# Kernel tuning notes

Hardware: AMD Instinct MI355X
Metric: run time of the kernel (lower is better)

The kernel has to match this reference:

```python
import jax, jax.numpy as jnp
import numpy as np

B, T, D, H, P, A = 128, 512, 512, 512, 512, 32  # envs, steps, feat, lstm hidden, latent, actions


def setup_inputs() -> dict:
    key = jax.random.key(0)
    ks = jax.random.split(key, 30)
    N = B * T
    lin = lambda k, o, i: 0.02 * jax.random.normal(k, (o, i), jnp.float32)
    vec = lambda k, o: 0.02 * jax.random.normal(k, (o,), jnp.float32)
    inp = {
        'features': jax.random.normal(ks[0], (N, D), jnp.float32),
        'episode_starts': (jax.random.uniform(ks[1], (N,)) < 0.02).astype(jnp.float32),
        'h0_pi': jax.random.normal(ks[2], (1, B, H), jnp.float32),
        'c0_pi': jax.random.normal(ks[3], (1, B, H), jnp.float32),
        'h0_vf': jax.random.normal(ks[4], (1, B, H), jnp.float32),
        'c0_vf': jax.random.normal(ks[5], (1, B, H), jnp.float32),
        'Wih_pi': lin(ks[6], 4 * H, D), 'Whh_pi': lin(ks[7], 4 * H, H),
        'bih_pi': vec(ks[8], 4 * H), 'bhh_pi': vec(ks[9], 4 * H),
        'Wih_vf': lin(ks[10], 4 * H, D), 'Whh_vf': lin(ks[11], 4 * H, H),
        'bih_vf': vec(ks[12], 4 * H), 'bhh_vf': vec(ks[13], 4 * H),
        'pol_w1': lin(ks[14], P, H), 'pol_b1': vec(ks[15], P),
        'pol_w2': lin(ks[16], P, P), 'pol_b2': vec(ks[17], P),
        'val_w1': lin(ks[18], P, H), 'val_b1': vec(ks[19], P),
        'val_w2': lin(ks[20], P, P), 'val_b2': vec(ks[21], P),
        'actor_w': lin(ks[22], A, P), 'actor_b': vec(ks[23], A),
        'critic_w': lin(ks[24], 1, P), 'critic_b': vec(ks[25], 1),
        'deterministic': 1,
    }
    return inp


def masked_lstm(xs, starts, h0, c0, Wih, Whh, bih, bhh):
    # xs: [T,B,D], starts: [T,B]; PyTorch gate order i,f,g,o; reset h,c where episode starts.
    def step(carry, inp):
        h, c = carry
        x, s = inp
        m = (1.0 - s)[:, None]
        h, c = h * m, c * m
        g = x @ Wih.T + bih + h @ Whh.T + bhh
        i, f, gg, o = jnp.split(g, 4, axis=-1)
        c = jax.nn.sigmoid(f) * c + jax.nn.sigmoid(i) * jnp.tanh(gg)
        h = jax.nn.sigmoid(o) * jnp.tanh(c)
        return (h, c), h
    (hT, cT), ys = jax.lax.scan(step, (h0[0], c0[0]), (xs, starts))
    return ys, hT[None], cT[None]


def mlp(x, w1, b1, w2, b2):
    return jax.nn.relu(x @ w1.T + b1) @ w2.T + b2


def reference(features, episode_starts, h0_pi, c0_pi, h0_vf, c0_vf,
              Wih_pi, Whh_pi, bih_pi, bhh_pi, Wih_vf, Whh_vf, bih_vf, bhh_vf,
              pol_w1, pol_b1, pol_w2, pol_b2, val_w1, val_b1, val_w2, val_b2,
              actor_w, actor_b, critic_w, critic_b, deterministic):
    n_seq = h0_pi.shape[1]
    d = features.shape[-1]
    xs = features.reshape(n_seq, -1, d).swapaxes(0, 1)        # [T,B,D]
    st = episode_starts.reshape(n_seq, -1).swapaxes(0, 1)     # [T,B]
    ys_pi, h_pi, c_pi = masked_lstm(xs, st, h0_pi, c0_pi, Wih_pi, Whh_pi, bih_pi, bhh_pi)
    ys_vf, h_vf, c_vf = masked_lstm(xs, st, h0_vf, c0_vf, Wih_vf, Whh_vf, bih_vf, bhh_vf)
    hsz = ys_pi.shape[-1]
    lat_pi = ys_pi.swapaxes(0, 1).reshape(-1, hsz)            # [B*T,H]
    lat_vf = ys_vf.swapaxes(0, 1).reshape(-1, hsz)
    lat_pi = mlp(lat_pi, pol_w1, pol_b1, pol_w2, pol_b2)
    lat_vf = mlp(lat_vf, val_w1, val_b1, val_w2, val_b2)
    values = lat_vf @ critic_w.T + critic_b                    # [B*T,1]
    logits = lat_pi @ actor_w.T + actor_b                      # [B*T,A]
    actions = jnp.argmax(logits, axis=-1)                      # deterministic mode
    logp = jax.nn.log_softmax(logits, axis=-1)
    log_prob = jnp.take_along_axis(logp, actions[:, None], axis=1)[:, 0]
    return actions, values, log_prob, h_pi, c_pi, h_vf, c_vf
```

## Files before the change

### kernel.cpp

```cpp
#include <hip/hip_runtime.h>
#include <math.h>

#define BB 128
#define TT 512
#define DD 512
#define HH 512
#define NN (BB*TT)
#define PP 512
#define AA 32
#define CH 64
#define CR (BB*CH)

typedef unsigned short u16;
typedef unsigned int   u32;
typedef __attribute__((ext_vector_type(8))) short short8;
typedef __attribute__((ext_vector_type(4))) float f32x4;

__device__ __forceinline__ u16 f2bf(float f){
    u32 x = __float_as_uint(f);
    u32 r = (x + 0x7fffu + ((x >> 16) & 1u)) >> 16;
    return (u16)r;
}
__device__ __forceinline__ float bf2f(u16 u){
    return __uint_as_float(((u32)u) << 16);
}
__device__ __forceinline__ f32x4 mfma16(short8 a, short8 b, f32x4 c){
    return __builtin_amdgcn_mfma_f32_16x16x32_bf16(a, b, c, 0, 0, 0);
}
__device__ __forceinline__ float sigm(float x){
    return 1.f/(1.f + __expf(-x));
}
__device__ __forceinline__ float tanh_f(float x){
    return 1.f - 2.f/(1.f + __expf(2.f*x));
}

__device__ __forceinline__ short8 ld_mall(const u16* p){
    short8 r;
    asm volatile("global_load_dwordx4 %0, %1, off sc0 sc1"
                 : "=&v"(r) : "v"(p) : "memory");
    return r;
}
__device__ __forceinline__ void st_mall(u16* p, short8 v){
    asm volatile("global_store_dwordx4 %0, %1, off sc0 sc1"
                 :: "v"(p), "v"(v) : "memory");
}

__device__ __forceinline__ unsigned a_add(unsigned* p){
    return __hip_atomic_fetch_add(p, 1u, __ATOMIC_RELAXED, __HIP_MEMORY_SCOPE_AGENT);
}
__device__ __forceinline__ unsigned a_ld(unsigned* p){
    return __hip_atomic_load(p, __ATOMIC_RELAXED, __HIP_MEMORY_SCOPE_AGENT);
}

#define BARZ_N 75264

__global__ __launch_bounds__(256) void prep_lstm_w(
    const float* __restrict__ Wih_pi, const float* __restrict__ Whh_pi,
    const float* __restrict__ bih_pi, const float* __restrict__ bhh_pi,
    const float* __restrict__ Wih_vf, const float* __restrict__ Whh_vf,
    const float* __restrict__ bih_vf, const float* __restrict__ bhh_vf,
    u16* __restrict__ wihHi, u16* __restrict__ wihLo,
    u16* __restrict__ whhHi, u16* __restrict__ whhLo,
    float* __restrict__ biasP)
{
    long i = (long)blockIdx.x*256 + threadIdx.x;
    if (i >= 2L*2048*512) return;
    int L = (int)(i >> 20);
    int rem = (int)(i & 1048575);
    int c = rem >> 9, k = rem & 511;
    int u = c >> 2, g = c & 3;
    long src = (long)(g*512 + u)*512 + k;
    float wih = (L ? Wih_vf : Wih_pi)[src];
    float whh = (L ? Whh_vf : Whh_pi)[src];
    u16 h1 = f2bf(wih); wihHi[i] = h1; wihLo[i] = f2bf(wih - bf2f(h1));
    u16 h2 = f2bf(whh); whhHi[i] = h2; whhLo[i] = f2bf(whh - bf2f(h2));
    if (k == 0) {
        float b = (L ? bih_vf : bih_pi)[g*512+u] + (L ? bhh_vf : bhh_pi)[g*512+u];
        biasP[L*2048 + c] = b;
    }
}

__global__ __launch_bounds__(256) void prep_mlp_w(
    const float* __restrict__ w1pi, const float* __restrict__ w1vf,
    const float* __restrict__ w2pi, const float* __restrict__ w2vf,
    const float* __restrict__ b1pi, const float* __restrict__ b1vf,
    const float* __restrict__ b2pi, const float* __restrict__ b2vf,
    u16* __restrict__ mHi, u16* __restrict__ mLo, float* __restrict__ biasM)
{
    long i = (long)blockIdx.x*256 + threadIdx.x;
    if (i >= 4L*262144) return;
    int mat = (int)(i >> 18);
    int rem = (int)(i & 262143);
    const float* src = mat==0 ? w1pi : mat==1 ? w1vf : mat==2 ? w2pi : w2vf;
    float v = src[rem];
    u16 h = f2bf(v); mHi[i] = h; mLo[i] = f2bf(v - bf2f(h));
    if (rem < 512) {
        const float* bs = mat==0 ? b1pi : mat==1 ? b1vf : mat==2 ? b2pi : b2vf;
        biasM[mat*512 + rem] = bs[rem];
    }
}

__global__ __launch_bounds__(256) void init_state_k(
    const float* __restrict__ h0_pi, const float* __restrict__ c0_pi,
    const float* __restrict__ h0_vf, const float* __restrict__ c0_vf,
    const float* __restrict__ starts,
    u16* __restrict__ hHi, u16* __restrict__ hLo, float* __restrict__ cT,
    float* __restrict__ startsT, unsigned* __restrict__ barZ)
{
    int i = blockIdx.x*256 + threadIdx.x;
    if (i < BARZ_N) barZ[i] = 0u;
    if (i < NN) {
        int e = i >> 9, t = i & 511;
        startsT[t*128 + e] = starts[i];
    }
    if (i >= 2*BB*HH) return;
    int L = i >> 16; int r = i & 65535;
    int e = r >> 9, u = r & 511;
    float m = 1.0f - starts[(long)e*TT];
    float h = (L ? h0_vf : h0_pi)[r] * m;
    float c = (L ? c0_vf : c0_pi)[r] * m;
    long hidx = (long)(L*2)*65536 + r;
    u16 hh = f2bf(h);
    hHi[hidx] = hh; hLo[hidx] = f2bf(h - bf2f(hh));
    cT[(long)L*65536 + (long)u*128 + e] = c;
}

template<int AM, int EM>
__global__ __launch_bounds__(256) void gemm_k512(
    const float* __restrict__ Afp,
    const u16* __restrict__ aHi, const u16* __restrict__ aLo, long aZ,
    int rowSh, int rowOuterHi, int rowOuterLo, int rowBase,
    const u16* __restrict__ bHi, const u16* __restrict__ bLo, long bZ,
    const float* __restrict__ bias, long biasZ,
    float* __restrict__ outF, long outFZ, int outLd,
    u16* __restrict__ oHi, u16* __restrict__ oLo, long oZ)
{
    __shared__ u16 sAh[5120], sAl[5120], sBh[5120], sBl[5120];
    const int tid = threadIdx.x;
    const int z = blockIdx.z;
    const long Mbase = (long)blockIdx.x * 128;
    const long Nbase = (long)blockIdx.y * 128;
    const int r2 = tid >> 1, half = tid & 1;
    const long mstage = Mbase + r2;
    const long arow = (mstage >> rowSh) * (long)rowOuterHi
                    + (mstage & (((long)1<<rowSh)-1)) * (long)rowOuterLo + rowBase;
    const long brow = Nbase + r2;
    const int wid = tid >> 6, lane = tid & 63;
    const int mh = wid & 1, nh = wid >> 1;
    const int l15 = lane & 15, quad = lane >> 4;

    f32x4 acc[4][4];
    #pragma unroll
    for (int i = 0; i < 4; ++i)
        #pragma unroll
        for (int j = 0; j < 4; ++j)
            acc[i][j] = (f32x4){0.f,0.f,0.f,0.f};

    const int sOffW = r2*40 + half*16;

    for (int kt = 0; kt < 16; ++kt) {
        const int k0 = kt*32;
        if constexpr (AM == 0) {
            const float* ap = Afp + arow*512 + k0 + half*16;
            float fv[16];
            #pragma unroll
            for (int q = 0; q < 4; ++q) *(float4*)(fv + q*4) = ((const float4*)ap)[q];
            short8 vh0, vh1, vl0, vl1;
            #pragma unroll
            for (int i = 0; i < 8; ++i){
                u16 h  = f2bf(fv[i]);   vh0[i] = (short)h;  vl0[i] = (short)f2bf(fv[i]   - bf2f(h));
                u16 h2 = f2bf(fv[8+i]); vh1[i] = (short)h2; vl1[i] = (short)f2bf(fv[8+i] - bf2f(h2));
            }
            *(short8*)(sAh + sOffW) = vh0; *(short8*)(sAh + sOffW + 8) = vh1;
            *(short8*)(sAl + sOffW) = vl0; *(short8*)(sAl + sOffW + 8) = vl1;
        } else {
            const u16* ph = aHi + (long)z*aZ + arow*512 + k0 + half*16;
            const u16* pl = aLo + (long)z*aZ + arow*512 + k0 + half*16;
            *(short8*)(sAh + sOffW) = *(const short8*)ph;
            *(short8*)(sAh + sOffW + 8) = *(const short8*)(ph + 8);
            *(short8*)(sAl + sOffW) = *(const short8*)pl;
            *(short8*)(sAl + sOffW + 8) = *(const short8*)(pl + 8);
        }
        {
            const u16* ph = bHi + (long)z*bZ + brow*512 + k0 + half*16;
            const u16* pl = bLo + (long)z*bZ + brow*512 + k0 + half*16;
            *(short8*)(sBh + sOffW) = *(const short8*)ph;
            *(short8*)(sBh + sOffW + 8) = *(const short8*)(ph + 8);
            *(short8*)(sBl + sOffW) = *(const short8*)pl;
            *(short8*)(sBl + sOffW + 8) = *(const short8*)(pl + 8);
        }
        __syncthreads();
        short8 bh[4], bl[4];
        #pragma unroll
        for (int nt = 0; nt < 4; ++nt){
            int bo = (nh*64 + nt*16 + l15)*40 + quad*8;
            bh[nt] = *(const short8*)(sBh + bo);
            bl[nt] = *(const short8*)(sBl + bo);
        }
        #pragma unroll
        for (int mt = 0; mt < 4; ++mt){
            int ao = (mh*64 + mt*16 + l15)*40 + quad*8;
            short8 ah = *(const short8*)(sAh + ao);
            short8 al = *(const short8*)(sAl + ao);
            #pragma unroll
            for (int nt = 0; nt < 4; ++nt){
                acc[mt][nt] = mfma16(ah, bh[nt], acc[mt][nt]);
                acc[mt][nt] = mfma16(ah, bl[nt], acc[mt][nt]);
                acc[mt][nt] = mfma16(al, bh[nt], acc[mt][nt]);
            }
        }
        __syncthreads();
    }
    #pragma unroll
    for (int nt = 0; nt < 4; ++nt){
        const long col = Nbase + nh*64 + nt*16 + l15;
        const float bv = bias[(long)z*biasZ + col];
        #pragma unroll
        for (int mt = 0; mt < 4; ++mt){
            const long rowm = Mbase + mh*64 + mt*16 + quad*4;
            #pragma unroll
            for (int rr = 0; rr < 4; ++rr){
                float v = acc[mt][nt][rr] + bv;
                const long m = rowm + rr;
                if constexpr (EM == 0) {
                    outF[(long)z*outFZ + m*(long)outLd + col] = v;
                } else {
                    if constexpr (EM == 1) v = fmaxf(v, 0.f);
                    u16 h = f2bf(v);
                    u16 l = f2bf(v - bf2f(h));
                    oHi[(long)z*oZ + m*512 + col] = h;
                    oLo[(long)z*oZ + m*512 + col] = l;
                }
            }
        }
    }
}

__global__ __launch_bounds__(256) void lstm_chunk(
    u16* __restrict__ hHi, u16* __restrict__ hLo,
    const u16* __restrict__ whhHi, const u16* __restrict__ whhLo,
    const float* __restrict__ gx,
    const float* __restrict__ startsT,
    float* __restrict__ cT,
    u16* __restrict__ ysHi, u16* __restrict__ ysLo,
    float* __restrict__ dout, unsigned* __restrict__ barZ, int t0)
{
    __shared__ __attribute__((aligned(16))) u16 sA[2][16384];
    __shared__ float zsm[4][144];
    __shared__ unsigned shLead, shNloc, shXC;

    const int tid  = threadIdx.x;
    const int wc   = blockIdx.x;
    const int eb   = blockIdx.y;
    const int L    = blockIdx.z;
    const int wid  = tid >> 6, lane = tid & 63;
    const int l15  = lane & 15, quad = lane >> 4;
    const int ebase = eb*64;
    const int e    = ebase + wid*16 + l15;

    unsigned xcc;
    asm("s_getreg_b32 %0, hwreg(HW_REG_XCC_ID)" : "=s"(xcc));
    xcc &= 7u;
    const int ch = t0 >> 6;
    unsigned* ARRb  = barZ;
    unsigned* DONEb = barZ + 65536;
    unsigned* RCNTb = barZ + 73728;
    unsigned* SBARb = barZ + 74752;
    unsigned* XCNTb = barZ + 74880;

    if (tid == 0){
        unsigned r = a_add(&RCNTb[(ch*8 + (int)xcc)*16]);
        shLead = (r == 0u) ? 1u : 0u;
        if (r == 0u){
            a_add(&XCNTb[ch*16]);
            asm volatile("s_waitcnt vmcnt(0)" ::: "memory");
        }
        a_add(&SBARb[ch*16]);
        while (a_ld(&SBARb[ch*16]) < 256u) __builtin_amdgcn_s_sleep(2);
        shNloc = a_ld(&RCNTb[(ch*8 + (int)xcc)*16]);
        shXC   = a_ld(&XCNTb[ch*16]);
    }

    {
        const size_t wbase = (size_t)L*1048576 + (size_t)(wc*32)*512;
        #pragma unroll
        for (int i = 0; i < 16; ++i){
            int f = tid + i*256;
            int pl = f >> 11;
            int r2 = f & 2047;
            int wcol = r2 >> 6, ksg = r2 & 63;
            const u16* src = (pl ? whhLo : whhHi) + wbase + (size_t)wcol*512 + ksg*8;
            int dst = (ksg>>2)*1024 + wcol*32 + (ksg&3)*8;
            *(short8*)(sA[pl] + dst) = *(const short8*)src;
        }
    }
    __syncthreads();
    const unsigned lead = shLead, nloc = shNloc, xcnt = shXC;

    const int u0 = wc*8 + quad;
    const int u1 = wc*8 + 4 + quad;
    const size_t ci0 = (size_t)L*65536 + (size_t)u0*128 + e;
    const size_t ci1 = (size_t)L*65536 + (size_t)u1*128 + e;
    float c0 = cT[ci0];
    float c1 = cT[ci1];

    const size_t hrowOff = (size_t)e*512 + quad*8;
    const size_t gxbase  = ((size_t)L*CR + e)*2048 + wc*32 + quad*4;

    for (int tau = 0; tau < CH; ++tau){
        const int t = t0 + tau;
        const int p = t & 1;

        const float* gp = gx + gxbase + (size_t)tau*(128*2048);
        float4 gv0 = *(const float4*)(gp);
        float4 gv1 = *(const float4*)(gp + 16);
        const float mn = (t < TT-1) ? (1.0f - startsT[(t+1)*128 + e]) : 1.0f;

        const u16* hHiP = hHi + (size_t)(L*2+p)*65536 + hrowOff;
        const u16* hLoP = hLo + (size_t)(L*2+p)*65536 + hrowOff;
        short8 pbh[4], pbl[4];
        #pragma unroll
        for (int i = 0; i < 4; ++i){
            pbh[i] = ld_mall(hHiP + i*32);
            pbl[i] = ld_mall(hLoP + i*32);
        }
        f32x4 acc0 = (f32x4){0.f,0.f,0.f,0.f};
        f32x4 acc1 = (f32x4){0.f,0.f,0.f,0.f};
        #pragma unroll
        for (int kt = 0; kt < 16; ++kt){
            if (kt < 13)      asm volatile("s_waitcnt vmcnt(6)" ::: "memory");
            else if (kt==13)  asm volatile("s_waitcnt vmcnt(4)" ::: "memory");
            else if (kt==14)  asm volatile("s_waitcnt vmcnt(2)" ::: "memory");
            else              asm volatile("s_waitcnt vmcnt(0)" ::: "memory");
            __builtin_amdgcn_sched_barrier(0);
            short8 bh = pbh[kt & 3];
            short8 bl = pbl[kt & 3];
            int a0 = kt*1024 + l15*32 + quad*8;
            short8 ah0 = *(const short8*)(sA[0] + a0);
            short8 al0 = *(const short8*)(sA[1] + a0);
            short8 ah1 = *(const short8*)(sA[0] + a0 + 512);
            short8 al1 = *(const short8*)(sA[1] + a0 + 512);
            acc0 = mfma16(ah0, bh, acc0);
            acc0 = mfma16(ah0, bl, acc0);
            acc0 = mfma16(al0, bh, acc0);
            acc1 = mfma16(ah1, bh, acc1);
            acc1 = mfma16(ah1, bl, acc1);
            acc1 = mfma16(al1, bh, acc1);
            if (kt < 12){
                pbh[kt & 3] = ld_mall(hHiP + (kt+4)*32);
                pbl[kt & 3] = ld_mall(hLoP + (kt+4)*32);
            }
        }

        {
            float ii = sigm(acc0[0] + gv0.x);
            float ff = sigm(acc0[1] + gv0.y);
            float gg = tanh_f(acc0[2] + gv0.z);
            float oo = sigm(acc0[3] + gv0.w);
            float cn = ff*c0 + ii*gg;
            float hn = oo * tanh_f(cn);
            c0 = cn * mn;
            zsm[wid][l15*8 + quad] = hn;
            zsm[wid][128 + l15] = mn;
            if (t == TT-1) {
                dout[(size_t)(3+2*L)*NN + (size_t)e*512 + u0] = hn;
                dout[(size_t)(4+2*L)*NN + (size_t)e*512 + u0] = cn;
            }
        }
        {
            float ii = sigm(acc1[0] + gv1.x);
            float ff = sigm(acc1[1] + gv1.y);
            float gg = tanh_f(acc1[2] + gv1.z);
            float oo = sigm(acc1[3] + gv1.w);
            float cn = ff*c1 + ii*gg;
            float hn = oo * tanh_f(cn);
            c1 = cn * mn;
            zsm[wid][l15*8 + 4 + quad] = hn;
            if (t == TT-1) {
                dout[(size_t)(3+2*L)*NN + (size_t)e*512 + u1] = hn;
                dout[(size_t)(4+2*L)*NN + (size_t)e*512 + u1] = cn;
            }
        }
        __syncthreads();

        {
            const int role = quad;
            const int e2 = l15;
            const int eg = ebase + wid*16 + e2;
            float v[8];
            #pragma unroll
            for (int j = 0; j < 8; ++j) v[j] = zsm[wid][e2*8 + j];
            const float mn2 = zsm[wid][128 + e2];
            short8 pk;
            if (role < 2) {
                #pragma unroll
                for (int j = 0; j < 8; ++j){
                    float hm = v[j] * mn2;
                    u16 h = f2bf(hm);
                    pk[j] = (short)(role == 0 ? h : f2bf(hm - bf2f(h)));
                }
                u16* dst = (role == 0 ? hHi : hLo)
                         + (size_t)(L*2 + (1-p))*65536 + (size_t)eg*512 + wc*8;
                st_mall(dst, pk);
            } else {
                #pragma unroll
                for (int j = 0; j < 8; ++j){
                    u16 h = f2bf(v[j]);
                    pk[j] = (short)(role == 2 ? h : f2bf(v[j] - bf2f(h)));
                }
                u16* dst = (role == 2 ? ysHi : ysLo)
                         + ((size_t)L*CR + (size_t)tau*128 + eg)*512 + wc*8;
                *(short8*)dst = pk;
            }
        }

        if (tau < CH-1){
            asm volatile("s_waitcnt vmcnt(0)" ::: "memory");
            __syncthreads();
            if (tid == 0){
                unsigned* ap = &ARRb[((size_t)t*8 + xcc)*16];
                unsigned* dp = &DONEb[(size_t)t*16];
                a_add(ap);
                if (lead){
                    while (a_ld(ap) < nloc) __builtin_amdgcn_s_sleep(1);
                    a_add(dp);
                }
                while (a_ld(dp) < xcnt) __builtin_amdgcn_s_sleep(1);
            }
            __syncthreads();
            asm volatile("" ::: "memory");
        }
    }

    cT[ci0] = c0;
    cT[ci1] = c1;
}

__global__ __launch_bounds__(256) void head_pi(
    const u16* __restrict__ latHi, const u16* __restrict__ latLo,
    const float* __restrict__ actor_w, const float* __restrict__ actor_b,
    float* __restrict__ dout, int t0)
{
    __shared__ float latS[16*516];
    __shared__ float lg[16*36];
    const int tid = threadIdx.x;
    const long r0 = (long)blockIdx.x * 16;
    {
        int rr = tid >> 4, seg = tid & 15;
        const u16* ph = latHi + (r0 + rr)*512 + seg*32;
        const u16* pl = latLo + (r0 + rr)*512 + seg*32;
        float* dst = latS + rr*516 + seg*32;
        #pragma unroll
        for (int ii = 0; ii < 4; ++ii){
            short8 vh = *(const short8*)(ph + ii*8);
            short8 vl = *(const short8*)(pl + ii*8);
            #pragma unroll
            for (int jj = 0; jj < 8; ++jj)
                dst[ii*8+jj] = bf2f((u16)vh[jj]) + bf2f((u16)vl[jj]);
        }
    }
    __syncthreads();
    {
        int rr = tid >> 4, a0 = (tid & 15)*2;
        const float4* lrow = (const float4*)(latS + rr*516);
        float acc0 = actor_b[a0], acc1 = actor_b[a0+1];
        for (int kq = 0; kq < 128; ++kq){
            float4 lv = lrow[kq];
            float4 w0 = ((const float4*)actor_w)[(a0  )*128 + kq];
            float4 w1 = ((const float4*)actor_w)[(a0+1)*128 + kq];
            acc0 += lv.x*w0.x + lv.y*w0.y + lv.z*w0.z + lv.w*w0.w;
            acc1 += lv.x*w1.x + lv.y*w1.y + lv.z*w1.z + lv.w*w1.w;
        }
        lg[rr*36 + a0]   = acc0;
        lg[rr*36 + a0+1] = acc1;
    }
    __syncthreads();
    if (tid < 16){
        float mx = -INFINITY; int am = 0;
        #pragma unroll
        for (int a = 0; a < AA; ++a){
            float v = lg[tid*36 + a];
            if (v > mx){ mx = v; am = a; }
        }
        float se = 0.f;
        #pragma unroll
        for (int a = 0; a < AA; ++a) se += expf(lg[tid*36 + a] - mx);
        long row = r0 + tid;
        long n = (row & 127)*TT + t0 + (row >> 7);
        dout[n] = (float)am;
        dout[2L*NN + n] = -logf(se);
    }
}

__global__ __launch_bounds__(256) void head_vf(
    const u16* __restrict__ latHi, const u16* __restrict__ latLo,
    const float* __restrict__ critic_w, const float* __restrict__ critic_b,
    float* __restrict__ dout, int t0)
{
    __shared__ float part[256];
    const int tid = threadIdx.x;
    const long r0 = (long)blockIdx.x * 32;
    int rr = tid >> 3, seg = tid & 7;
    const u16* ph = latHi + (r0 + rr)*512 + seg*64;
    const u16* pl = latLo + (r0 + rr)*512 + seg*64;
    float acc = 0.f;
    #pragma unroll
    for (int ii = 0; ii < 8; ++ii){
        short8 vh = *(const short8*)(ph + ii*8);
        short8 vl = *(const short8*)(pl + ii*8);
        #pragma unroll
        for (int jj = 0; jj < 8; ++jj){
            float lv = bf2f((u16)vh[jj]) + bf2f((u16)vl[jj]);
            acc += lv * critic_w[seg*64 + ii*8 + jj];
        }
    }
    part[tid] = acc;
    __syncthreads();
    if (tid < 32){
        float v = critic_b[0];
        #pragma unroll
        for (int s = 0; s < 8; ++s) v += part[tid*8 + s];
        long row = r0 + tid;
        long n = (row & 127)*TT + t0 + (row >> 7);
        dout[(long)NN + n] = v;
    }
}

extern "C" void kernel_launch(void* const* d_in, const int* in_sizes, int n_in,
                              void* d_out, int out_size, void* d_ws, size_t ws_size,
                              hipStream_t stream) {
    const float* features = (const float*)d_in[0];
    const float* starts   = (const float*)d_in[1];
    const float* h0_pi = (const float*)d_in[2];
    const float* c0_pi = (const float*)d_in[3];
    const float* h0_vf = (const float*)d_in[4];
    const float* c0_vf = (const float*)d_in[5];
    const float* Wih_pi = (const float*)d_in[6];
    const float* Whh_pi = (const float*)d_in[7];
    const float* bih_pi = (const float*)d_in[8];
    const float* bhh_pi = (const float*)d_in[9];
    const float* Wih_vf = (const float*)d_in[10];
    const float* Whh_vf = (const float*)d_in[11];
    const float* bih_vf = (const float*)d_in[12];
    const float* bhh_vf = (const float*)d_in[13];
    const float* pol_w1 = (const float*)d_in[14];
    const float* pol_b1 = (const float*)d_in[15];
    const float* pol_w2 = (const float*)d_in[16];
    const float* pol_b2 = (const float*)d_in[17];
    const float* val_w1 = (const float*)d_in[18];
    const float* val_b1 = (const float*)d_in[19];
    const float* val_w2 = (const float*)d_in[20];
    const float* val_b2 = (const float*)d_in[21];
    const float* actor_w  = (const float*)d_in[22];
    const float* actor_b  = (const float*)d_in[23];
    const float* critic_w = (const float*)d_in[24];
    const float* critic_b = (const float*)d_in[25];
    float* out = (float*)d_out;

    size_t off = 0;
    auto alloc = [&](size_t b) {
        void* p = (char*)d_ws + off;
        off += (b + 255) & ~(size_t)255;
        return p;
    };
    u16* wihHi = (u16*)alloc(2L*2048*512*2);
    u16* wihLo = (u16*)alloc(2L*2048*512*2);
    u16* whhHi = (u16*)alloc(2L*2048*512*2);
    u16* whhLo = (u16*)alloc(2L*2048*512*2);
    float* biasP = (float*)alloc(2L*2048*4);
    u16* mHi = (u16*)alloc(4L*262144*2);
    u16* mLo = (u16*)alloc(4L*262144*2);
    float* biasM = (float*)alloc(4L*512*4);
    u16* hHi = (u16*)alloc(2L*2*128*512*2);
    u16* hLo = (u16*)alloc(2L*2*128*512*2);
    float* cT  = (float*)alloc(2L*128*512*4);
    float* startsT = (float*)alloc((size_t)NN*4);
    unsigned* barZ = (unsigned*)alloc((size_t)BARZ_N*4);
    u16* ysHi = (u16*)alloc(2L*CR*512*2);
    u16* ysLo = (u16*)alloc(2L*CR*512*2);
    u16* hidHi = (u16*)alloc(2L*CR*512*2);
    u16* hidLo = (u16*)alloc(2L*CR*512*2);
    u16* latHi = (u16*)alloc(2L*CR*512*2);
    u16* latLo = (u16*)alloc(2L*CR*512*2);
    float* gxF = (float*)alloc(2L*CR*2048*4);
    const long gxZ = (long)CR*2048;
    const long pZ  = (long)CR*512;

    prep_lstm_w<<<dim3(8192), dim3(256), 0, stream>>>(
        Wih_pi, Whh_pi, bih_pi, bhh_pi, Wih_vf, Whh_vf, bih_vf, bhh_vf,
        wihHi, wihLo, whhHi, whhLo, biasP);
    prep_mlp_w<<<dim3(4096), dim3(256), 0, stream>>>(
        pol_w1, val_w1, pol_w2, val_w2, pol_b1, val_b1, pol_b2, val_b2,
        mHi, mLo, biasM);
    init_state_k<<<dim3(512), dim3(256), 0, stream>>>(
        h0_pi, c0_pi, h0_vf, c0_vf, starts, hHi, hLo, cT, startsT, barZ);

    for (int t0 = 0; t0 < TT; t0 += CH) {
        gemm_k512<0,0><<<dim3(CR/128, 16, 2), dim3(256), 0, stream>>>(
            features, nullptr, nullptr, 0L,
            7, 1, 512, t0,
            wihHi, wihLo, 1048576L,
            biasP, 2048L,
            gxF, gxZ, 2048,
            nullptr, nullptr, 0L);
        lstm_chunk<<<dim3(64, 2, 2), dim3(256), 0, stream>>>(
            hHi, hLo, whhHi, whhLo, gxF, startsT, cT, ysHi, ysLo,
            out, barZ, t0);
        gemm_k512<1,1><<<dim3(CR/128, 4, 2), dim3(256), 0, stream>>>(
            nullptr, ysHi, ysLo, pZ,
            30, 0, 1, 0,
            mHi, mLo, 262144L,
            biasM, 512L,
            nullptr, 0L, 0,
            hidHi, hidLo, pZ);
        gemm_k512<1,2><<<dim3(CR/128, 4, 2), dim3(256), 0, stream>>>(
            nullptr, hidHi, hidLo, pZ,
            30, 0, 1, 0,
            mHi + 2L*262144, mLo + 2L*262144, 262144L,
            biasM + 1024, 512L,
            nullptr, 0L, 0,
            latHi, latLo, pZ);
        head_pi<<<dim3(CR/16), dim3(256), 0, stream>>>(
            latHi, latLo, actor_w, actor_b, out, t0);
        head_vf<<<dim3(CR/32), dim3(256), 0, stream>>>(
            latHi + pZ, latLo + pZ, critic_w, critic_b, out, t0);
    }
}
```

Before: 6.816 ms.

## Issue all h loads upfront and prefetch next-step gates during grid barrier

Each LSTM step now issues all 16 h-fragment loads at once and waits in four coarse groups, replacing the rolling 4-deep prefetch. The next step's gx gate values and reset mask are loaded while the grid-wide arrival/done spin-wait runs, taking them off the critical path. Only the h-state stores wait on vmcnt; the ys stores do not. The writeback role is now split by wave instead of by lane quad, and __syncthreads becomes a raw s_barrier. This raises register pressure from 32 in-flight short8 buffers, and relies on the per-wave vmcnt wait plus s_barrier being enough to order the h stores before the arrival signal.

```diff
diff --git a/kernel.cpp b/kernel.cpp
--- a/kernel.cpp
+++ b/kernel.cpp
@@ -307,20 +307,19 @@
     const size_t hrowOff = (size_t)e*512 + quad*8;
     const size_t gxbase  = ((size_t)L*CR + e)*2048 + wc*32 + quad*4;
 
+    float4 gv0 = *(const float4*)(gx + gxbase);
+    float4 gv1 = *(const float4*)(gx + gxbase + 16);
+    float mn = (t0 < TT-1) ? (1.0f - startsT[(t0+1)*128 + e]) : 1.0f;
+
     for (int tau = 0; tau < CH; ++tau){
         const int t = t0 + tau;
         const int p = t & 1;
 
-        const float* gp = gx + gxbase + (size_t)tau*(128*2048);
-        float4 gv0 = *(const float4*)(gp);
-        float4 gv1 = *(const float4*)(gp + 16);
-        const float mn = (t < TT-1) ? (1.0f - startsT[(t+1)*128 + e]) : 1.0f;
-
         const u16* hHiP = hHi + (size_t)(L*2+p)*65536 + hrowOff;
         const u16* hLoP = hLo + (size_t)(L*2+p)*65536 + hrowOff;
-        short8 pbh[4], pbl[4];
-        #pragma unroll
-        for (int i = 0; i < 4; ++i){
+        short8 pbh[16], pbl[16];
+        #pragma unroll
+        for (int i = 0; i < 16; ++i){
             pbh[i] = ld_mall(hHiP + i*32);
             pbl[i] = ld_mall(hLoP + i*32);
         }
@@ -328,13 +327,21 @@
         f32x4 acc1 = (f32x4){0.f,0.f,0.f,0.f};
         #pragma unroll
         for (int kt = 0; kt < 16; ++kt){
-            if (kt < 13)      asm volatile("s_waitcnt vmcnt(6)" ::: "memory");
-            else if (kt==13)  asm volatile("s_waitcnt vmcnt(4)" ::: "memory");
-            else if (kt==14)  asm volatile("s_waitcnt vmcnt(2)" ::: "memory");
-            else              asm volatile("s_waitcnt vmcnt(0)" ::: "memory");
-            __builtin_amdgcn_sched_barrier(0);
-            short8 bh = pbh[kt & 3];
-            short8 bl = pbl[kt & 3];
+            if (kt == 0){
+                asm volatile("s_waitcnt vmcnt(24)" ::: "memory");
+                __builtin_amdgcn_sched_barrier(0);
+            } else if (kt == 4){
+                asm volatile("s_waitcnt vmcnt(16)" ::: "memory");
+                __builtin_amdgcn_sched_barrier(0);
+            } else if (kt == 8){
+                asm volatile("s_waitcnt vmcnt(8)" ::: "memory");
+                __builtin_amdgcn_sched_barrier(0);
+            } else if (kt == 12){
+                asm volatile("s_waitcnt vmcnt(0)" ::: "memory");
+                __builtin_amdgcn_sched_barrier(0);
+            }
+            short8 bh = pbh[kt];
+            short8 bl = pbl[kt];
             int a0 = kt*1024 + l15*32 + quad*8;
             short8 ah0 = *(const short8*)(sA[0] + a0);
             short8 al0 = *(const short8*)(sA[1] + a0);
@@ -346,10 +353,6 @@
             acc1 = mfma16(ah1, bh, acc1);
             acc1 = mfma16(ah1, bl, acc1);
             acc1 = mfma16(al1, bh, acc1);
-            if (kt < 12){
-                pbh[kt & 3] = ld_mall(hHiP + (kt+4)*32);
-                pbl[kt & 3] = ld_mall(hLoP + (kt+4)*32);
-            }
         }
 
         {
@@ -384,50 +387,54 @@
         __syncthreads();
 
         {
-            const int role = quad;
+            const int g2 = quad;
             const int e2 = l15;
-            const int eg = ebase + wid*16 + e2;
+            const int eg = ebase + g2*16 + e2;
             float v[8];
             #pragma unroll
-            for (int j = 0; j < 8; ++j) v[j] = zsm[wid][e2*8 + j];
-            const float mn2 = zsm[wid][128 + e2];
+            for (int j = 0; j < 8; ++j) v[j] = zsm[g2][e2*8 + j];
+            const float mn2 = zsm[g2][128 + e2];
             short8 pk;
-            if (role < 2) {
+            if (wid < 2) {
                 #pragma unroll
                 for (int j = 0; j < 8; ++j){
                     float hm = v[j] * mn2;
                     u16 h = f2bf(hm);
-                    pk[j] = (short)(role == 0 ? h : f2bf(hm - bf2f(h)));
+                    pk[j] = (short)(wid == 0 ? h : f2bf(hm - bf2f(h)));
                 }
-                u16* dst = (role == 0 ? hHi : hLo)
+                u16* dst = (wid == 0 ? hHi : hLo)
                          + (size_t)(L*2 + (1-p))*65536 + (size_t)eg*512 + wc*8;
                 st_mall(dst, pk);
+                asm volatile("s_waitcnt vmcnt(0)" ::: "memory");
             } else {
                 #pragma unroll
                 for (int j = 0; j < 8; ++j){
                     u16 h = f2bf(v[j]);
-                    pk[j] = (short)(role == 2 ? h : f2bf(v[j] - bf2f(h)));
+                    pk[j] = (short)(wid == 2 ? h : f2bf(v[j] - bf2f(h)));
                 }
-                u16* dst = (role == 2 ? ysHi : ysLo)
+                u16* dst = (wid == 2 ? ysHi : ysLo)
                          + ((size_t)L*CR + (size_t)tau*128 + eg)*512 + wc*8;
                 *(short8*)dst = pk;
             }
         }
 
+        __builtin_amdgcn_s_barrier();
         if (tau < CH-1){
-            asm volatile("s_waitcnt vmcnt(0)" ::: "memory");
-            __syncthreads();
+            if (tid == 0) a_add(&ARRb[((size_t)t*8 + xcc)*16]);
+            const float* gpn = gx + gxbase + (size_t)(tau+1)*(128*2048);
+            gv0 = *(const float4*)(gpn);
+            gv1 = *(const float4*)(gpn + 16);
+            mn = (t+1 < TT-1) ? (1.0f - startsT[(t+2)*128 + e]) : 1.0f;
             if (tid == 0){
                 unsigned* ap = &ARRb[((size_t)t*8 + xcc)*16];
                 unsigned* dp = &DONEb[(size_t)t*16];
-                a_add(ap);
                 if (lead){
                     while (a_ld(ap) < nloc) __builtin_amdgcn_s_sleep(1);
                     a_add(dp);
                 }
                 while (a_ld(dp) < xcnt) __builtin_amdgcn_s_sleep(1);
             }
-            __syncthreads();
+            __builtin_amdgcn_s_barrier();
             asm volatile("" ::: "memory");
         }
     }
```

Measured after the change: 6.713 ms. No clear change (-1.5%).
